# Kernel optimization log

Measured on AMD Instinct MI355X. Metric: run time of the kernel, lower is better.

## Reference

```python
import jax, jax.numpy as jnp
import numpy as np

B, T = 2, 20
IMG, P, C = 224, 16, 3
DIM, DEPTH, HEADS, DH, MLP = 768, 12, 12, 64, 3072
NPATCH = (IMG // P) ** 2  # 196
INNER = HEADS * DH  # 768


def setup_inputs() -> dict:
    key = jax.random.key(0)
    ks = jax.random.split(key, 24)
    std = 0.02
    inp = {
        'img': jax.random.normal(ks[0], (B, T, C, IMG, IMG), jnp.float32),
        'face': jax.random.normal(ks[1], (B * T, 2, DIM), jnp.float32),
        'conv_w': jax.random.normal(ks[2], (DIM, C, P, P), jnp.float32) * std,
        'conv_b': jnp.zeros((DIM,), jnp.float32),
        'pos_emb': jax.random.normal(ks[3], (1, NPATCH + 1, DIM), jnp.float32),
        'time_emb': jax.random.normal(ks[4], (T, DIM), jnp.float32) * std,
        'cls_tok': jax.random.normal(ks[5], (1, 1, DIM), jnp.float32),
        'ln1_s': jnp.ones((DEPTH, DIM), jnp.float32),
        'ln1_b': jnp.zeros((DEPTH, DIM), jnp.float32),
        'qkv_w': jax.random.normal(ks[6], (DEPTH, DIM, 3 * INNER), jnp.float32) * std,
        'out_w': jax.random.normal(ks[7], (DEPTH, INNER, DIM), jnp.float32) * std,
        'out_b': jnp.zeros((DEPTH, DIM), jnp.float32),
        'ln2_s': jnp.ones((DEPTH, DIM), jnp.float32),
        'ln2_b': jnp.zeros((DEPTH, DIM), jnp.float32),
        'ff_w1': jax.random.normal(ks[8], (DEPTH, DIM, MLP), jnp.float32) * std,
        'ff_b1': jnp.zeros((DEPTH, MLP), jnp.float32),
        'ff_w2': jax.random.normal(ks[9], (DEPTH, MLP, DIM), jnp.float32) * std,
        'ff_b2': jnp.zeros((DEPTH, DIM), jnp.float32),
    }
    return inp


def _ln(x, s, b):
    m = x.mean(-1, keepdims=True)
    v = ((x - m) ** 2).mean(-1, keepdims=True)
    return (x - m) / jnp.sqrt(v + 1e-5) * s + b


def _vit_forward(img, face, conv_w, conv_b, pos_emb, time_emb, cls_tok,
                 ln1_s, ln1_b, qkv_w, out_w, out_b, ln2_s, ln2_b,
                 ff_w1, ff_b1, ff_w2, ff_b2):
    Bv, Tv = img.shape[0], img.shape[1]
    bt = Bv * Tv
    x = img.reshape(bt, C, IMG, IMG)
    # conv patch embed, kernel == stride == P
    x = jax.lax.conv_general_dilated(x, conv_w, (P, P), 'VALID',
                                     dimension_numbers=('NCHW', 'OIHW', 'NCHW'))
    x = x + conv_b[None, :, None, None]
    x = x.reshape(bt, DIM, -1).transpose(0, 2, 1)  # (bt, 196, dim)
    n = x.shape[1]
    cls = jnp.broadcast_to(cls_tok, (bt, 1, DIM))
    x = jnp.concatenate([cls, x], axis=1) + pos_emb[:, :n + 1]
    x = jnp.concatenate([x, face], axis=1)  # (bt, 199, dim)
    ntok = x.shape[1]
    # temporal encoding (T == time_embed rows)
    x = (x.reshape(Bv, Tv, ntok, DIM) + time_emb[None, :, None, :]).reshape(bt, ntok, DIM)
    scale = DH ** -0.5
    for i in range(DEPTH):
        h = _ln(x, ln1_s[i], ln1_b[i])
        qkv = h @ qkv_w[i]
        q, k, v = jnp.split(qkv, 3, axis=-1)
        def heads(t):
            return t.reshape(bt, ntok, HEADS, DH).transpose(0, 2, 1, 3)
        q, k, v = heads(q), heads(k), heads(v)
        dots = jnp.einsum('bhid,bhjd->bhij', q, k) * scale
        attn = jax.nn.softmax(dots, axis=-1)
        o = jnp.einsum('bhij,bhjd->bhid', attn, v)
        o = o.transpose(0, 2, 1, 3).reshape(bt, ntok, INNER)
        x = x + (o @ out_w[i] + out_b[i])
        h = _ln(x, ln2_s[i], ln2_b[i])
        f = jax.nn.gelu(h @ ff_w1[i] + ff_b1[i], approximate=False) @ ff_w2[i] + ff_b2[i]
        x = x + f
    return (x[:, 0, :], x[:, -2, :], x[:, -1, :], x[:, 1:-2, :])


def reference(img, face, conv_w, conv_b, pos_emb, time_emb, cls_tok,
              ln1_s, ln1_b, qkv_w, out_w, out_b, ln2_s, ln2_b,
              ff_w1, ff_b1, ff_w2, ff_b2):
    return _vit_forward(img, face, conv_w, conv_b, pos_emb, time_emb, cls_tok,
                        ln1_s, ln1_b, qkv_w, out_w, out_b, ln2_s, ln2_b,
                        ff_w1, ff_b1, ff_w2, ff_b2)
```

## Files before the change

### kernel.cpp

```cpp
#include <hip/hip_runtime.h>
#include <math.h>

constexpr int BB = 2, TT = 20;
constexpr int IMG = 224, PATCH = 16, CH = 3;
constexpr int DIM = 768, DEPTH = 12, HEADS = 12, DH = 64, MLP = 3072;
constexpr int NPATCH = 196;
constexpr int NTOK = 199;
constexpr int BT = BB * TT;
constexpr int MROWS = BT * NTOK;
constexpr int INNER = HEADS * DH;
constexpr int QKVDIM = 3 * INNER;

__device__ __forceinline__ float gelu_f(float x) {
    return 0.5f * x * (1.0f + erff(x * 0.70710678118654752f));
}

__global__ void im2col_k(const float* __restrict__ img, float* __restrict__ A) {
    int idx = blockIdx.x * 256 + threadIdx.x;
    int k = idx % 768;
    int m = idx / 768;
    int bt = m / NPATCH, p = m % NPATCH;
    int c = k >> 8;
    int r = k & 255;
    int ph = r >> 4, pw = r & 15;
    int py = p / 14, px = p % 14;
    A[idx] = img[(((size_t)bt * CH + c) * IMG + (py * 16 + ph)) * IMG + (px * 16 + pw)];
}

template <int EPI, bool BTL>
__global__ __launch_bounds__(256) void gemm_k(
        const float* __restrict__ A, const float* __restrict__ B,
        const float* __restrict__ bias, float* __restrict__ C,
        int Mm, int N, int K) {
    __shared__ float As[16][132];
    __shared__ float Bs[16][132];

    const int tid = threadIdx.x;
    const int m0 = blockIdx.y * 128;
    const int n0 = blockIdx.x * 128;
    const int ty = tid >> 4;
    const int tx = tid & 15;

    float acc[8][8];
#pragma unroll
    for (int i = 0; i < 8; ++i)
#pragma unroll
        for (int j = 0; j < 8; ++j) acc[i][j] = 0.f;

    const int a_m = tid >> 2;
    const int a_k4 = (tid & 3) * 4;
    const int b_k = tid >> 5;
    const int b_n4 = (tid & 31) * 4;

    for (int k0 = 0; k0 < K; k0 += 16) {
#pragma unroll
        for (int pass = 0; pass < 2; ++pass) {
            int m = m0 + a_m + pass * 64;
            float4 v = make_float4(0.f, 0.f, 0.f, 0.f);
            if (m < Mm)
                v = *reinterpret_cast<const float4*>(A + (size_t)m * K + k0 + a_k4);
            int ml = a_m + pass * 64;
            As[a_k4 + 0][ml] = v.x;
            As[a_k4 + 1][ml] = v.y;
            As[a_k4 + 2][ml] = v.z;
            As[a_k4 + 3][ml] = v.w;
        }
        if (!BTL) {
#pragma unroll
            for (int pass = 0; pass < 2; ++pass) {
                int k = b_k + pass * 8;
                float4 v = *reinterpret_cast<const float4*>(
                    B + (size_t)(k0 + k) * N + n0 + b_n4);
                *reinterpret_cast<float4*>(&Bs[k][b_n4]) = v;
            }
        } else {
#pragma unroll
            for (int pass = 0; pass < 2; ++pass) {
                int n = n0 + a_m + pass * 64;
                float4 v = *reinterpret_cast<const float4*>(
                    B + (size_t)n * K + k0 + a_k4);
                int nl = a_m + pass * 64;
                Bs[a_k4 + 0][nl] = v.x;
                Bs[a_k4 + 1][nl] = v.y;
                Bs[a_k4 + 2][nl] = v.z;
                Bs[a_k4 + 3][nl] = v.w;
            }
        }
        __syncthreads();

#pragma unroll
        for (int k = 0; k < 16; ++k) {
            float4 a0 = *reinterpret_cast<const float4*>(&As[k][ty * 8]);
            float4 a1 = *reinterpret_cast<const float4*>(&As[k][ty * 8 + 4]);
            float4 b0 = *reinterpret_cast<const float4*>(&Bs[k][tx * 8]);
            float4 b1 = *reinterpret_cast<const float4*>(&Bs[k][tx * 8 + 4]);
            float av[8] = {a0.x, a0.y, a0.z, a0.w, a1.x, a1.y, a1.z, a1.w};
            float bv[8] = {b0.x, b0.y, b0.z, b0.w, b1.x, b1.y, b1.z, b1.w};
#pragma unroll
            for (int i = 0; i < 8; ++i)
#pragma unroll
                for (int j = 0; j < 8; ++j) acc[i][j] += av[i] * bv[j];
        }
        __syncthreads();
    }

#pragma unroll
    for (int i = 0; i < 8; ++i) {
        int m = m0 + ty * 8 + i;
        if (m < Mm) {
            float* crow = C + (size_t)m * N + n0 + tx * 8;
#pragma unroll
            for (int jj = 0; jj < 2; ++jj) {
                float4 o;
                if (EPI == 0) {
                    o.x = acc[i][jj * 4 + 0];
                    o.y = acc[i][jj * 4 + 1];
                    o.z = acc[i][jj * 4 + 2];
                    o.w = acc[i][jj * 4 + 3];
                } else if (EPI == 1) {
                    float4 bz = *reinterpret_cast<const float4*>(bias + n0 + tx * 8 + jj * 4);
                    float4 r = *reinterpret_cast<const float4*>(crow + jj * 4);
                    o.x = acc[i][jj * 4 + 0] + bz.x + r.x;
                    o.y = acc[i][jj * 4 + 1] + bz.y + r.y;
                    o.z = acc[i][jj * 4 + 2] + bz.z + r.z;
                    o.w = acc[i][jj * 4 + 3] + bz.w + r.w;
                } else {
                    float4 bz = *reinterpret_cast<const float4*>(bias + n0 + tx * 8 + jj * 4);
                    o.x = gelu_f(acc[i][jj * 4 + 0] + bz.x);
                    o.y = gelu_f(acc[i][jj * 4 + 1] + bz.y);
                    o.z = gelu_f(acc[i][jj * 4 + 2] + bz.z);
                    o.w = gelu_f(acc[i][jj * 4 + 3] + bz.w);
                }
                *reinterpret_cast<float4*>(crow + jj * 4) = o;
            }
        }
    }
}

__global__ void assemble_k(const float* __restrict__ Xc, const float* __restrict__ face,
                           const float* __restrict__ conv_b, const float* __restrict__ pos,
                           const float* __restrict__ time_emb, const float* __restrict__ cls,
                           float* __restrict__ X) {
    int idx = blockIdx.x * 256 + threadIdx.x;
    int d = idx % DIM;
    int tok = (idx / DIM) % NTOK;
    int bt = idx / (DIM * NTOK);
    int t = bt % TT;
    float v;
    if (tok == 0) {
        v = cls[d] + pos[d];
    } else if (tok <= NPATCH) {
        v = Xc[((size_t)bt * NPATCH + (tok - 1)) * DIM + d] + conv_b[d] + pos[tok * DIM + d];
    } else {
        v = face[((size_t)bt * 2 + (tok - NPATCH - 1)) * DIM + d];
    }
    v += time_emb[t * DIM + d];
    X[idx] = v;
}

__global__ __launch_bounds__(64) void ln_k(const float* __restrict__ X,
                                           const float* __restrict__ s,
                                           const float* __restrict__ b,
                                           float* __restrict__ out) {
    int row = blockIdx.x;
    int lane = threadIdx.x;
    const float4* xr = reinterpret_cast<const float4*>(X + (size_t)row * DIM);
    float4 v0 = xr[lane], v1 = xr[lane + 64], v2 = xr[lane + 128];
    float sum = v0.x + v0.y + v0.z + v0.w + v1.x + v1.y + v1.z + v1.w +
                v2.x + v2.y + v2.z + v2.w;
#pragma unroll
    for (int off = 32; off; off >>= 1) sum += __shfl_xor(sum, off);
    float mean = sum * (1.f / DIM);
    float sq = 0.f;
#pragma unroll
    for (int c = 0; c < 3; ++c) {
        float4 v = (c == 0) ? v0 : (c == 1) ? v1 : v2;
        float dx = v.x - mean, dy = v.y - mean, dz = v.z - mean, dw = v.w - mean;
        sq += dx * dx + dy * dy + dz * dz + dw * dw;
    }
#pragma unroll
    for (int off = 32; off; off >>= 1) sq += __shfl_xor(sq, off);
    float var = sq * (1.f / DIM);
    float rstd = rsqrtf(var + 1e-5f);
    const float4* sr = reinterpret_cast<const float4*>(s);
    const float4* br = reinterpret_cast<const float4*>(b);
    float4* orow = reinterpret_cast<float4*>(out + (size_t)row * DIM);
#pragma unroll
    for (int c = 0; c < 3; ++c) {
        float4 v = (c == 0) ? v0 : (c == 1) ? v1 : v2;
        float4 sc = sr[lane + 64 * c];
        float4 bc = br[lane + 64 * c];
        float4 o;
        o.x = (v.x - mean) * rstd * sc.x + bc.x;
        o.y = (v.y - mean) * rstd * sc.y + bc.y;
        o.z = (v.z - mean) * rstd * sc.z + bc.z;
        o.w = (v.w - mean) * rstd * sc.w + bc.w;
        orow[lane + 64 * c] = o;
    }
}

__global__ __launch_bounds__(64) void attn_k(const float* __restrict__ qkv,
                                             float* __restrict__ O) {
    int i = blockIdx.x;
    int h = blockIdx.y;
    int bt = blockIdx.z;
    int lane = threadIdx.x;

    __shared__ __align__(16) float qsh[DH];
    __shared__ float psh[NTOK + 1];

    const float* base = qkv + (size_t)bt * NTOK * QKVDIM;
    qsh[lane] = base[(size_t)i * QKVDIM + h * DH + lane];
    __syncthreads();

    const float4* q4 = reinterpret_cast<const float4*>(qsh);
    float vals[4];
    float mx = -1e30f;
#pragma unroll
    for (int r = 0; r < 4; ++r) {
        int j = lane + 64 * r;
        vals[r] = -1e30f;
        if (j < NTOK) {
            const float4* kr = reinterpret_cast<const float4*>(
                base + (size_t)j * QKVDIM + INNER + h * DH);
            float d = 0.f;
#pragma unroll
            for (int kk = 0; kk < 16; ++kk) {
                float4 kv = kr[kk];
                float4 qv = q4[kk];
                d += qv.x * kv.x + qv.y * kv.y + qv.z * kv.z + qv.w * kv.w;
            }
            vals[r] = d * 0.125f;
        }
        mx = fmaxf(mx, vals[r]);
    }
#pragma unroll
    for (int off = 32; off; off >>= 1) mx = fmaxf(mx, __shfl_xor(mx, off));

    float ssum = 0.f;
#pragma unroll
    for (int r = 0; r < 4; ++r) {
        int j = lane + 64 * r;
        if (j < NTOK) {
            float e = expf(vals[r] - mx);
            ssum += e;
            psh[j] = e;
        }
    }
#pragma unroll
    for (int off = 32; off; off >>= 1) ssum += __shfl_xor(ssum, off);
    float inv = 1.f / ssum;
    __syncthreads();

    float o = 0.f;
    const float* vbase = base + 2 * INNER + h * DH + lane;
    for (int j = 0; j < NTOK; ++j) {
        o += psh[j] * vbase[(size_t)j * QKVDIM];
    }
    O[((size_t)bt * NTOK + i) * DIM + h * DH + lane] = o * inv;
}

__global__ void out_k(const float* __restrict__ X, float* __restrict__ out) {
    int idx = blockIdx.x * 256 + threadIdx.x;
    const int R = BT * DIM;
    float v;
    if (idx < R) {
        int bt = idx / DIM, d = idx % DIM;
        v = X[((size_t)bt * NTOK + 0) * DIM + d];
    } else if (idx < 2 * R) {
        int r = idx - R;
        int bt = r / DIM, d = r % DIM;
        v = X[((size_t)bt * NTOK + 197) * DIM + d];
    } else if (idx < 3 * R) {
        int r = idx - 2 * R;
        int bt = r / DIM, d = r % DIM;
        v = X[((size_t)bt * NTOK + 198) * DIM + d];
    } else {
        int r = idx - 3 * R;
        int bt = r / (NPATCH * DIM);
        int rem = r % (NPATCH * DIM);
        int tok = rem / DIM + 1;
        int d = rem % DIM;
        v = X[((size_t)bt * NTOK + tok) * DIM + d];
    }
    out[idx] = v;
}

extern "C" void kernel_launch(void* const* d_in, const int* in_sizes, int n_in,
                              void* d_out, int out_size, void* d_ws, size_t ws_size,
                              hipStream_t stream) {
    const float* img      = (const float*)d_in[0];
    const float* face     = (const float*)d_in[1];
    const float* conv_w   = (const float*)d_in[2];
    const float* conv_b   = (const float*)d_in[3];
    const float* pos_emb  = (const float*)d_in[4];
    const float* time_emb = (const float*)d_in[5];
    const float* cls_tok  = (const float*)d_in[6];
    const float* ln1_s    = (const float*)d_in[7];
    const float* ln1_b    = (const float*)d_in[8];
    const float* qkv_w    = (const float*)d_in[9];
    const float* out_w    = (const float*)d_in[10];
    const float* out_b    = (const float*)d_in[11];
    const float* ln2_s    = (const float*)d_in[12];
    const float* ln2_b    = (const float*)d_in[13];
    const float* ff_w1    = (const float*)d_in[14];
    const float* ff_b1    = (const float*)d_in[15];
    const float* ff_w2    = (const float*)d_in[16];
    const float* ff_w2b   = (const float*)d_in[17];
    float* outp = (float*)d_out;

    const size_t XSZ = (size_t)BT * NTOK * DIM;
    float* X   = (float*)d_ws;
    float* H   = X + XSZ;
    float* O   = H + XSZ;
    float* TMP = O + XSZ;
    float* Aim = TMP;
    float* Xc  = TMP + (size_t)BT * NPATCH * DIM;
    float* QKV = TMP;
    float* F   = TMP;

    const int PM = BT * NPATCH;

    im2col_k<<<(PM * DIM) / 256, 256, 0, stream>>>(img, Aim);
    {
        dim3 g(DIM / 128, (PM + 127) / 128);
        gemm_k<0, true><<<g, 256, 0, stream>>>(Aim, conv_w, nullptr, Xc, PM, DIM, DIM);
    }
    assemble_k<<<(BT * NTOK * DIM) / 256, 256, 0, stream>>>(
        Xc, face, conv_b, pos_emb, time_emb, cls_tok, X);

    for (int l = 0; l < DEPTH; ++l) {
        ln_k<<<MROWS, 64, 0, stream>>>(X, ln1_s + l * DIM, ln1_b + l * DIM, H);
        {
            dim3 g(QKVDIM / 128, (MROWS + 127) / 128);
            gemm_k<0, false><<<g, 256, 0, stream>>>(
                H, qkv_w + (size_t)l * DIM * QKVDIM, nullptr, QKV, MROWS, QKVDIM, DIM);
        }
        {
            dim3 g(NTOK, HEADS, BT);
            attn_k<<<g, 64, 0, stream>>>(QKV, O);
        }
        {
            dim3 g(DIM / 128, (MROWS + 127) / 128);
            gemm_k<1, false><<<g, 256, 0, stream>>>(
                O, out_w + (size_t)l * INNER * DIM, out_b + l * DIM, X, MROWS, DIM, INNER);
        }
        ln_k<<<MROWS, 64, 0, stream>>>(X, ln2_s + l * DIM, ln2_b + l * DIM, H);
        {
            dim3 g(MLP / 128, (MROWS + 127) / 128);
            gemm_k<2, false><<<g, 256, 0, stream>>>(
                H, ff_w1 + (size_t)l * DIM * MLP, ff_b1 + l * MLP, F, MROWS, MLP, DIM);
        }
        {
            dim3 g(DIM / 128, (MROWS + 127) / 128);
            gemm_k<1, false><<<g, 256, 0, stream>>>(
                F, ff_w2 + (size_t)l * MLP * DIM, ff_w2b + l * DIM, X, MROWS, DIM, MLP);
        }
    }

    out_k<<<(BT * NTOK * DIM) / 256, 256, 0, stream>>>(X, outp);
}
```

Measured before the change: 28.18 ms.

## Switch GEMMs to bf16 MFMA and restructure attention per head block

Replaces the fp32 SIMT GEMM with a bf16 MFMA 16x16x32 kernel. Weights are transposed and cast to bf16 each layer, and LayerNorm, attention output and the GELU activations are stored as bf16. Attention is rewritten so one block per (batch, head) loads K and V into shared memory once and processes all queries, where before each query reloaded K and V from global memory. This cuts FLOP cost and memory traffic, at the price of bf16 precision loss and extra per-layer weight transpose kernels.

```diff
diff --git a/kernel.cpp b/kernel.cpp
--- a/kernel.cpp
+++ b/kernel.cpp
@@ -1,4 +1,5 @@
 #include <hip/hip_runtime.h>
+#include <hip/hip_bf16.h>
 #include <math.h>
 
 constexpr int BB = 2, TT = 20;
@@ -11,11 +12,36 @@
 constexpr int INNER = HEADS * DH;
 constexpr int QKVDIM = 3 * INNER;
 
+typedef short bf16x8 __attribute__((ext_vector_type(8)));
+typedef float f32x4 __attribute__((ext_vector_type(4)));
+
+__device__ __forceinline__ ushort f2bf(float x) {
+    __hip_bfloat16 h = __float2bfloat16(x);
+    return *reinterpret_cast<ushort*>(&h);
+}
 __device__ __forceinline__ float gelu_f(float x) {
     return 0.5f * x * (1.0f + erff(x * 0.70710678118654752f));
 }
 
-__global__ void im2col_k(const float* __restrict__ img, float* __restrict__ A) {
+__global__ void tr_k(const float* __restrict__ W, ushort* __restrict__ Wt, int K, int N) {
+    __shared__ float t[32][33];
+    int n0 = blockIdx.x * 32, k0 = blockIdx.y * 32;
+    int tx = threadIdx.x, ty = threadIdx.y;
+#pragma unroll
+    for (int p = 0; p < 4; ++p)
+        t[ty + 8 * p][tx] = W[(size_t)(k0 + ty + 8 * p) * N + n0 + tx];
+    __syncthreads();
+#pragma unroll
+    for (int p = 0; p < 4; ++p)
+        Wt[(size_t)(n0 + ty + 8 * p) * K + k0 + tx] = f2bf(t[tx][ty + 8 * p]);
+}
+
+__global__ void cast_k(const float* __restrict__ in, ushort* __restrict__ out, int n) {
+    int i = blockIdx.x * 256 + threadIdx.x;
+    if (i < n) out[i] = f2bf(in[i]);
+}
+
+__global__ void im2col_k(const float* __restrict__ img, ushort* __restrict__ A) {
     int idx = blockIdx.x * 256 + threadIdx.x;
     int k = idx % 768;
     int m = idx / 768;
@@ -24,114 +50,88 @@
     int r = k & 255;
     int ph = r >> 4, pw = r & 15;
     int py = p / 14, px = p % 14;
-    A[idx] = img[(((size_t)bt * CH + c) * IMG + (py * 16 + ph)) * IMG + (px * 16 + pw)];
-}
-
-template <int EPI, bool BTL>
-__global__ __launch_bounds__(256) void gemm_k(
-        const float* __restrict__ A, const float* __restrict__ B,
-        const float* __restrict__ bias, float* __restrict__ C,
+    A[idx] = f2bf(img[(((size_t)bt * CH + c) * IMG + (py * 16 + ph)) * IMG + (px * 16 + pw)]);
+}
+
+template <int EPI>
+__global__ __launch_bounds__(256) void mgemm_k(
+        const ushort* __restrict__ A, const ushort* __restrict__ Bt,
+        const float* __restrict__ bias, void* __restrict__ Cv,
         int Mm, int N, int K) {
-    __shared__ float As[16][132];
-    __shared__ float Bs[16][132];
-
+    __shared__ __align__(16) ushort As[128 * 40];
+    __shared__ __align__(16) ushort Bs[128 * 40];
     const int tid = threadIdx.x;
-    const int m0 = blockIdx.y * 128;
-    const int n0 = blockIdx.x * 128;
-    const int ty = tid >> 4;
-    const int tx = tid & 15;
-
-    float acc[8][8];
-#pragma unroll
-    for (int i = 0; i < 8; ++i)
-#pragma unroll
-        for (int j = 0; j < 8; ++j) acc[i][j] = 0.f;
-
-    const int a_m = tid >> 2;
-    const int a_k4 = (tid & 3) * 4;
-    const int b_k = tid >> 5;
-    const int b_n4 = (tid & 31) * 4;
-
-    for (int k0 = 0; k0 < K; k0 += 16) {
-#pragma unroll
-        for (int pass = 0; pass < 2; ++pass) {
-            int m = m0 + a_m + pass * 64;
-            float4 v = make_float4(0.f, 0.f, 0.f, 0.f);
-            if (m < Mm)
-                v = *reinterpret_cast<const float4*>(A + (size_t)m * K + k0 + a_k4);
-            int ml = a_m + pass * 64;
-            As[a_k4 + 0][ml] = v.x;
-            As[a_k4 + 1][ml] = v.y;
-            As[a_k4 + 2][ml] = v.z;
-            As[a_k4 + 3][ml] = v.w;
-        }
-        if (!BTL) {
-#pragma unroll
-            for (int pass = 0; pass < 2; ++pass) {
-                int k = b_k + pass * 8;
-                float4 v = *reinterpret_cast<const float4*>(
-                    B + (size_t)(k0 + k) * N + n0 + b_n4);
-                *reinterpret_cast<float4*>(&Bs[k][b_n4]) = v;
-            }
-        } else {
-#pragma unroll
-            for (int pass = 0; pass < 2; ++pass) {
-                int n = n0 + a_m + pass * 64;
-                float4 v = *reinterpret_cast<const float4*>(
-                    B + (size_t)n * K + k0 + a_k4);
-                int nl = a_m + pass * 64;
-                Bs[a_k4 + 0][nl] = v.x;
-                Bs[a_k4 + 1][nl] = v.y;
-                Bs[a_k4 + 2][nl] = v.z;
-                Bs[a_k4 + 3][nl] = v.w;
-            }
+    const int l = tid & 63, w = tid >> 6;
+    const int wr = w >> 1, wc = w & 1;
+    const int g = l >> 4, r = l & 15;
+    const int m0 = blockIdx.y * 128, n0 = blockIdx.x * 128;
+
+    f32x4 acc[4][4];
+#pragma unroll
+    for (int i = 0; i < 4; ++i)
+#pragma unroll
+        for (int j = 0; j < 4; ++j) acc[i][j] = (f32x4){0.f, 0.f, 0.f, 0.f};
+
+    const int srow = tid >> 1;
+    const int c0 = (tid & 1) * 2;
+    const bool aval = (m0 + srow) < Mm;
+    const ushort* aptr = A + (size_t)(m0 + srow) * K;
+    const ushort* bptr = Bt + (size_t)(n0 + srow) * K;
+
+    for (int kt = 0; kt < K; kt += 32) {
+        int4 ra[2], rb[2];
+#pragma unroll
+        for (int p = 0; p < 2; ++p) {
+            int c = c0 + p;
+            ra[p] = aval ? *reinterpret_cast<const int4*>(aptr + kt + 8 * c)
+                         : make_int4(0, 0, 0, 0);
+            rb[p] = *reinterpret_cast<const int4*>(bptr + kt + 8 * c);
         }
         __syncthreads();
-
-#pragma unroll
-        for (int k = 0; k < 16; ++k) {
-            float4 a0 = *reinterpret_cast<const float4*>(&As[k][ty * 8]);
-            float4 a1 = *reinterpret_cast<const float4*>(&As[k][ty * 8 + 4]);
-            float4 b0 = *reinterpret_cast<const float4*>(&Bs[k][tx * 8]);
-            float4 b1 = *reinterpret_cast<const float4*>(&Bs[k][tx * 8 + 4]);
-            float av[8] = {a0.x, a0.y, a0.z, a0.w, a1.x, a1.y, a1.z, a1.w};
-            float bv[8] = {b0.x, b0.y, b0.z, b0.w, b1.x, b1.y, b1.z, b1.w};
-#pragma unroll
-            for (int i = 0; i < 8; ++i)
-#pragma unroll
-                for (int j = 0; j < 8; ++j) acc[i][j] += av[i] * bv[j];
+#pragma unroll
+        for (int p = 0; p < 2; ++p) {
+            int c = c0 + p;
+            int base = srow * 40 + 8 * c;
+            *reinterpret_cast<int4*>(&As[base]) = ra[p];
+            *reinterpret_cast<int4*>(&Bs[base]) = rb[p];
         }
         __syncthreads();
-    }
-
-#pragma unroll
-    for (int i = 0; i < 8; ++i) {
-        int m = m0 + ty * 8 + i;
-        if (m < Mm) {
-            float* crow = C + (size_t)m * N + n0 + tx * 8;
-#pragma unroll
-            for (int jj = 0; jj < 2; ++jj) {
-                float4 o;
-                if (EPI == 0) {
-                    o.x = acc[i][jj * 4 + 0];
-                    o.y = acc[i][jj * 4 + 1];
-                    o.z = acc[i][jj * 4 + 2];
-                    o.w = acc[i][jj * 4 + 3];
-                } else if (EPI == 1) {
-                    float4 bz = *reinterpret_cast<const float4*>(bias + n0 + tx * 8 + jj * 4);
-                    float4 r = *reinterpret_cast<const float4*>(crow + jj * 4);
-                    o.x = acc[i][jj * 4 + 0] + bz.x + r.x;
-                    o.y = acc[i][jj * 4 + 1] + bz.y + r.y;
-                    o.z = acc[i][jj * 4 + 2] + bz.z + r.z;
-                    o.w = acc[i][jj * 4 + 3] + bz.w + r.w;
-                } else {
-                    float4 bz = *reinterpret_cast<const float4*>(bias + n0 + tx * 8 + jj * 4);
-                    o.x = gelu_f(acc[i][jj * 4 + 0] + bz.x);
-                    o.y = gelu_f(acc[i][jj * 4 + 1] + bz.y);
-                    o.z = gelu_f(acc[i][jj * 4 + 2] + bz.z);
-                    o.w = gelu_f(acc[i][jj * 4 + 3] + bz.w);
+
+        bf16x8 af[4], bfr[4];
+#pragma unroll
+        for (int fi = 0; fi < 4; ++fi)
+            af[fi] = *reinterpret_cast<const bf16x8*>(&As[(wr * 64 + fi * 16 + r) * 40 + g * 8]);
+#pragma unroll
+        for (int fj = 0; fj < 4; ++fj)
+            bfr[fj] = *reinterpret_cast<const bf16x8*>(&Bs[(wc * 64 + fj * 16 + r) * 40 + g * 8]);
+#pragma unroll
+        for (int fi = 0; fi < 4; ++fi)
+#pragma unroll
+            for (int fj = 0; fj < 4; ++fj)
+                acc[fi][fj] = __builtin_amdgcn_mfma_f32_16x16x32_bf16(
+                    af[fi], bfr[fj], acc[fi][fj], 0, 0, 0);
+    }
+
+    float* Cf = (float*)Cv;
+    ushort* Cu = (ushort*)Cv;
+#pragma unroll
+    for (int fi = 0; fi < 4; ++fi) {
+#pragma unroll
+        for (int e = 0; e < 4; ++e) {
+            int row = m0 + wr * 64 + fi * 16 + g * 4 + e;
+            if (row < Mm) {
+#pragma unroll
+                for (int fj = 0; fj < 4; ++fj) {
+                    int col = n0 + wc * 64 + fj * 16 + r;
+                    float v = acc[fi][fj][e];
+                    if (EPI == 0) {
+                        Cf[(size_t)row * N + col] = v;
+                    } else if (EPI == 1) {
+                        Cf[(size_t)row * N + col] += v + bias[col];
+                    } else {
+                        Cu[(size_t)row * N + col] = f2bf(gelu_f(v + bias[col]));
+                    }
                 }
-                *reinterpret_cast<float4*>(crow + jj * 4) = o;
             }
         }
     }
@@ -161,7 +161,7 @@
 __global__ __launch_bounds__(64) void ln_k(const float* __restrict__ X,
                                            const float* __restrict__ s,
                                            const float* __restrict__ b,
-                                           float* __restrict__ out) {
+                                           ushort* __restrict__ out) {
     int row = blockIdx.x;
     int lane = threadIdx.x;
     const float4* xr = reinterpret_cast<const float4*>(X + (size_t)row * DIM);
@@ -180,84 +180,129 @@
     }
 #pragma unroll
     for (int off = 32; off; off >>= 1) sq += __shfl_xor(sq, off);
-    float var = sq * (1.f / DIM);
-    float rstd = rsqrtf(var + 1e-5f);
+    float rstd = rsqrtf(sq * (1.f / DIM) + 1e-5f);
     const float4* sr = reinterpret_cast<const float4*>(s);
     const float4* br = reinterpret_cast<const float4*>(b);
-    float4* orow = reinterpret_cast<float4*>(out + (size_t)row * DIM);
+    ushort4* orow = reinterpret_cast<ushort4*>(out + (size_t)row * DIM);
 #pragma unroll
     for (int c = 0; c < 3; ++c) {
         float4 v = (c == 0) ? v0 : (c == 1) ? v1 : v2;
         float4 sc = sr[lane + 64 * c];
         float4 bc = br[lane + 64 * c];
-        float4 o;
-        o.x = (v.x - mean) * rstd * sc.x + bc.x;
-        o.y = (v.y - mean) * rstd * sc.y + bc.y;
-        o.z = (v.z - mean) * rstd * sc.z + bc.z;
-        o.w = (v.w - mean) * rstd * sc.w + bc.w;
+        ushort4 o;
+        o.x = f2bf((v.x - mean) * rstd * sc.x + bc.x);
+        o.y = f2bf((v.y - mean) * rstd * sc.y + bc.y);
+        o.z = f2bf((v.z - mean) * rstd * sc.z + bc.z);
+        o.w = f2bf((v.w - mean) * rstd * sc.w + bc.w);
         orow[lane + 64 * c] = o;
     }
 }
 
-__global__ __launch_bounds__(64) void attn_k(const float* __restrict__ qkv,
-                                             float* __restrict__ O) {
-    int i = blockIdx.x;
-    int h = blockIdx.y;
-    int bt = blockIdx.z;
-    int lane = threadIdx.x;
-
-    __shared__ __align__(16) float qsh[DH];
-    __shared__ float psh[NTOK + 1];
-
+__global__ __launch_bounds__(256) void attn_k(const float* __restrict__ qkv,
+                                              ushort* __restrict__ O) {
+    __shared__ __align__(16) float Kl[256][68];
+    __shared__ __align__(16) float Vt[64][204];
+    __shared__ __align__(16) float Qs[4][4][68];
+    __shared__ __align__(16) float Ps[4][4][208];
+
+    const int h = blockIdx.x % HEADS;
+    const int bt = blockIdx.x / HEADS;
+    const int tid = threadIdx.x, l = tid & 63, w = tid >> 6;
     const float* base = qkv + (size_t)bt * NTOK * QKVDIM;
-    qsh[lane] = base[(size_t)i * QKVDIM + h * DH + lane];
+
+    for (int it = 0; it < 50; ++it) {
+        int idx = tid + it * 256;
+        int j = idx >> 6, d = idx & 63;
+        if (j < NTOK) {
+            Kl[j][d] = base[(size_t)j * QKVDIM + INNER + h * DH + d];
+            Vt[d][j] = base[(size_t)j * QKVDIM + 2 * INNER + h * DH + d];
+        }
+    }
+    if (tid < 64) {
+        Vt[tid][199] = 0.f; Vt[tid][200] = 0.f; Vt[tid][201] = 0.f;
+        Vt[tid][202] = 0.f; Vt[tid][203] = 0.f;
+    }
     __syncthreads();
 
-    const float4* q4 = reinterpret_cast<const float4*>(qsh);
-    float vals[4];
-    float mx = -1e30f;
-#pragma unroll
-    for (int r = 0; r < 4; ++r) {
-        int j = lane + 64 * r;
-        vals[r] = -1e30f;
-        if (j < NTOK) {
-            const float4* kr = reinterpret_cast<const float4*>(
-                base + (size_t)j * QKVDIM + INNER + h * DH);
-            float d = 0.f;
-#pragma unroll
-            for (int kk = 0; kk < 16; ++kk) {
-                float4 kv = kr[kk];
-                float4 qv = q4[kk];
-                d += qv.x * kv.x + qv.y * kv.y + qv.z * kv.z + qv.w * kv.w;
-            }
-            vals[r] = d * 0.125f;
-        }
-        mx = fmaxf(mx, vals[r]);
-    }
-#pragma unroll
-    for (int off = 32; off; off >>= 1) mx = fmaxf(mx, __shfl_xor(mx, off));
-
-    float ssum = 0.f;
-#pragma unroll
-    for (int r = 0; r < 4; ++r) {
-        int j = lane + 64 * r;
-        if (j < NTOK) {
-            float e = expf(vals[r] - mx);
-            ssum += e;
-            psh[j] = e;
-        }
-    }
-#pragma unroll
-    for (int off = 32; off; off >>= 1) ssum += __shfl_xor(ssum, off);
-    float inv = 1.f / ssum;
-    __syncthreads();
-
-    float o = 0.f;
-    const float* vbase = base + 2 * INNER + h * DH + lane;
-    for (int j = 0; j < NTOK; ++j) {
-        o += psh[j] * vbase[(size_t)j * QKVDIM];
-    }
-    O[((size_t)bt * NTOK + i) * DIM + h * DH + lane] = o * inv;
+    const int qp = l >> 4;
+    const int qq = l & 15;
+
+    for (int G = w; G < 50; G += 4) {
+        const int ibase = G * 4;
+        {
+            int i = min(ibase + qp, NTOK - 1);
+            float4 qv = *reinterpret_cast<const float4*>(
+                base + (size_t)i * QKVDIM + h * DH + qq * 4);
+            *reinterpret_cast<float4*>(&Qs[w][qp][qq * 4]) = qv;
+        }
+        float acc[4][4];
+#pragma unroll
+        for (int p = 0; p < 4; ++p)
+#pragma unroll
+            for (int kc = 0; kc < 4; ++kc) acc[p][kc] = 0.f;
+
+#pragma unroll
+        for (int kk = 0; kk < 16; ++kk) {
+            float4 q4[4];
+#pragma unroll
+            for (int p = 0; p < 4; ++p)
+                q4[p] = *reinterpret_cast<const float4*>(&Qs[w][p][kk * 4]);
+#pragma unroll
+            for (int kc = 0; kc < 4; ++kc) {
+                int j = l + 64 * kc;
+                float4 k4 = *reinterpret_cast<const float4*>(&Kl[j][kk * 4]);
+#pragma unroll
+                for (int p = 0; p < 4; ++p)
+                    acc[p][kc] += q4[p].x * k4.x + q4[p].y * k4.y +
+                                  q4[p].z * k4.z + q4[p].w * k4.w;
+            }
+        }
+        float pexp[4][4];
+#pragma unroll
+        for (int p = 0; p < 4; ++p) {
+            float mx = -1e30f;
+#pragma unroll
+            for (int kc = 0; kc < 4; ++kc) {
+                int j = l + 64 * kc;
+                float sc = (j < NTOK) ? acc[p][kc] * 0.125f : -1e30f;
+                acc[p][kc] = sc;
+                mx = fmaxf(mx, sc);
+            }
+#pragma unroll
+            for (int off = 32; off; off >>= 1) mx = fmaxf(mx, __shfl_xor(mx, off));
+            float ss = 0.f;
+#pragma unroll
+            for (int kc = 0; kc < 4; ++kc) {
+                float e = __expf(acc[p][kc] - mx);
+                pexp[p][kc] = e;
+                ss += e;
+            }
+#pragma unroll
+            for (int off = 32; off; off >>= 1) ss += __shfl_xor(ss, off);
+            float inv = 1.f / ss;
+#pragma unroll
+            for (int kc = 0; kc < 4; ++kc) {
+                int j = l + 64 * kc;
+                if (j < 200) Ps[w][p][j] = pexp[p][kc] * inv;
+            }
+        }
+        float o[4] = {0.f, 0.f, 0.f, 0.f};
+#pragma unroll
+        for (int jq = 0; jq < 50; ++jq) {
+            float4 v4 = *reinterpret_cast<const float4*>(&Vt[l][jq * 4]);
+#pragma unroll
+            for (int p = 0; p < 4; ++p) {
+                float4 p4 = *reinterpret_cast<const float4*>(&Ps[w][p][jq * 4]);
+                o[p] += p4.x * v4.x + p4.y * v4.y + p4.z * v4.z + p4.w * v4.w;
+            }
+        }
+#pragma unroll
+        for (int p = 0; p < 4; ++p) {
+            int i = ibase + p;
+            if (i < NTOK)
+                O[((size_t)bt * NTOK + i) * DIM + h * DH + l] = f2bf(o[p]);
+        }
+    }
 }
 
 __global__ void out_k(const float* __restrict__ X, float* __restrict__ out) {
@@ -309,52 +354,62 @@
     const float* ff_w2b   = (const float*)d_in[17];
     float* outp = (float*)d_out;
 
-    const size_t XSZ = (size_t)BT * NTOK * DIM;
-    float* X   = (float*)d_ws;
-    float* H   = X + XSZ;
-    float* O   = H + XSZ;
-    float* TMP = O + XSZ;
-    float* Aim = TMP;
-    float* Xc  = TMP + (size_t)BT * NPATCH * DIM;
-    float* QKV = TMP;
-    float* F   = TMP;
+    const size_t XSZ = (size_t)MROWS * DIM;
+    const size_t HSLOT = XSZ / 2;
+    float* X    = (float*)d_ws;
+    ushort* H   = (ushort*)(X + XSZ);
+    ushort* Ob  = (ushort*)(X + XSZ + HSLOT);
+    float* TMP  = X + XSZ + 2 * HSLOT;
+    float* QKV  = TMP;
+    ushort* F   = (ushort*)TMP;
+    ushort* Aim = (ushort*)TMP;
+    float* Xc   = TMP + 3010560;
+    float* WEND = TMP + (size_t)MROWS * QKVDIM;
+    ushort* WqT = (ushort*)WEND;
+    ushort* WoT = WqT + 2304 * 768;
+    ushort* W1T = WoT + 768 * 768;
+    ushort* W2T = W1T + 3072 * 768;
+    ushort* CW  = W2T + 768 * 3072;
 
     const int PM = BT * NPATCH;
 
+    cast_k<<<(768 * 768 + 255) / 256, 256, 0, stream>>>(conv_w, CW, 768 * 768);
     im2col_k<<<(PM * DIM) / 256, 256, 0, stream>>>(img, Aim);
     {
         dim3 g(DIM / 128, (PM + 127) / 128);
-        gemm_k<0, true><<<g, 256, 0, stream>>>(Aim, conv_w, nullptr, Xc, PM, DIM, DIM);
+        mgemm_k<0><<<g, 256, 0, stream>>>(Aim, CW, nullptr, Xc, PM, DIM, DIM);
     }
     assemble_k<<<(BT * NTOK * DIM) / 256, 256, 0, stream>>>(
         Xc, face, conv_b, pos_emb, time_emb, cls_tok, X);
 
     for (int l = 0; l < DEPTH; ++l) {
+        tr_k<<<dim3(QKVDIM / 32, DIM / 32), dim3(32, 8), 0, stream>>>(
+            qkv_w + (size_t)l * DIM * QKVDIM, WqT, DIM, QKVDIM);
+        tr_k<<<dim3(DIM / 32, INNER / 32), dim3(32, 8), 0, stream>>>(
+            out_w + (size_t)l * INNER * DIM, WoT, INNER, DIM);
+        tr_k<<<dim3(MLP / 32, DIM / 32), dim3(32, 8), 0, stream>>>(
+            ff_w1 + (size_t)l * DIM * MLP, W1T, DIM, MLP);
+        tr_k<<<dim3(DIM / 32, MLP / 32), dim3(32, 8), 0, stream>>>(
+            ff_w2 + (size_t)l * MLP * DIM, W2T, MLP, DIM);
+
         ln_k<<<MROWS, 64, 0, stream>>>(X, ln1_s + l * DIM, ln1_b + l * DIM, H);
         {
             dim3 g(QKVDIM / 128, (MROWS + 127) / 128);
-            gemm_k<0, false><<<g, 256, 0, stream>>>(
-                H, qkv_w + (size_t)l * DIM * QKVDIM, nullptr, QKV, MROWS, QKVDIM, DIM);
-        }
-        {
-            dim3 g(NTOK, HEADS, BT);
-            attn_k<<<g, 64, 0, stream>>>(QKV, O);
-        }
+            mgemm_k<0><<<g, 256, 0, stream>>>(H, WqT, nullptr, QKV, MROWS, QKVDIM, DIM);
+        }
+        attn_k<<<BT * HEADS, 256, 0, stream>>>(QKV, Ob);
         {
             dim3 g(DIM / 128, (MROWS + 127) / 128);
-            gemm_k<1, false><<<g, 256, 0, stream>>>(
-                O, out_w + (size_t)l * INNER * DIM, out_b + l * DIM, X, MROWS, DIM, INNER);
+            mgemm_k<1><<<g, 256, 0, stream>>>(Ob, WoT, out_b + l * DIM, X, MROWS, DIM, INNER);
         }
         ln_k<<<MROWS, 64, 0, stream>>>(X, ln2_s + l * DIM, ln2_b + l * DIM, H);
         {
             dim3 g(MLP / 128, (MROWS + 127) / 128);
-            gemm_k<2, false><<<g, 256, 0, stream>>>(
-                H, ff_w1 + (size_t)l * DIM * MLP, ff_b1 + l * MLP, F, MROWS, MLP, DIM);
+            mgemm_k<2><<<g, 256, 0, stream>>>(H, W1T, ff_b1 + l * MLP, F, MROWS, MLP, DIM);
         }
         {
             dim3 g(DIM / 128, (MROWS + 127) / 128);
-            gemm_k<1, false><<<g, 256, 0, stream>>>(
-                F, ff_w2 + (size_t)l * MLP * DIM, ff_w2b + l * DIM, X, MROWS, DIM, MLP);
+            mgemm_k<1><<<g, 256, 0, stream>>>(F, W2T, ff_w2b + l * DIM, X, MROWS, DIM, MLP);
         }
     }
 
```

Result: faster. 23.68 ms (-16.0%).
